# Kernel tuning notes

Hardware: AMD Instinct MI355X
Metric: run time of the kernel (lower is better)

The kernel has to match this reference:

```python
import jax, jax.numpy as jnp
import numpy as np
from jax import lax

WINDOW = 40          # plan.window_size
E = 8                # len(plan.expand_feature)
F = 64               # len(plan.feature)
OUT_CH = 128
KERNEL = 5
ALPHA = 0.01         # leaky_relu_alpha
N_LABEL = 1


def time_conv(x, conv_size):
    """x: [N, T, F] -> [N, WINDOW, 5*E] sliding-window stats over first E features."""
    N, T, _ = x.shape
    begin = T - (conv_size + WINDOW - 1)
    xe = x[:, :, :E]                                             # [N, T, E]
    idx = begin + jnp.arange(WINDOW)[:, None] + jnp.arange(conv_size)[None, :]  # [W, C]
    win = xe[:, idx, :]                                          # [N, W, C, E]
    _mean = win.mean(axis=2)                                     # [N, W, E]
    _std = jnp.std(win, axis=2, ddof=1)                          # torch.std is unbiased
    _max = win.max(axis=2)
    _min = win.min(axis=2)
    # rank of last timestep of each window, cross-sectionally over stocks (dim 0)
    last = xe[:, begin + conv_size - 1: begin + conv_size - 1 + WINDOW, :]  # [N, W, E]
    order = jnp.argsort(-last, axis=0)
    rank = jnp.argsort(order, axis=0).astype(x.dtype) / N        # [N, W, E]
    return jnp.concatenate([_mean, _std, rank, _max, _min], axis=2)  # [N, W, 5E]


def setup_inputs() -> dict:
    key = jax.random.key(0)
    k1, k2, k3, k4, k5 = jax.random.split(key, 5)
    N, T = 8000, 64
    in_ch = F + 10 * E  # 144
    x = jax.random.normal(k1, (N, T, F), dtype=jnp.float32)
    conv_w = jax.random.normal(k2, (OUT_CH, in_ch, KERNEL), dtype=jnp.float32) * 0.05
    conv_b = jax.random.normal(k3, (OUT_CH,), dtype=jnp.float32) * 0.05
    lin_in = WINDOW + 1 - KERNEL  # 36
    lin_w = jax.random.normal(k4, (N_LABEL, lin_in), dtype=jnp.float32) * 0.1
    lin_b = jax.random.normal(k5, (N_LABEL,), dtype=jnp.float32) * 0.1
    return {"x": x, "conv_w": conv_w, "conv_b": conv_b, "lin_w": lin_w, "lin_b": lin_b}


def reference(x, conv_w, conv_b, lin_w, lin_b):
    week_x = time_conv(x, conv_size=5)     # [N, W, 5E]
    month_x = time_conv(x, conv_size=20)   # [N, W, 5E]
    xc = jnp.concatenate([x[:, -WINDOW:, :], week_x, month_x], axis=2)  # [N, W, F+10E]
    cnn_x = jnp.transpose(xc, (0, 2, 1))   # [N, C, W]
    part = lax.conv_general_dilated(cnn_x, conv_w, window_strides=(1,),
                                    padding='VALID',
                                    dimension_numbers=('NCH', 'OIH', 'NCH'))
    part = part + conv_b[None, :, None]    # [N, OUT_CH, W+1-K]
    h = part[:, -1, :]                     # last output channel, [N, W+1-K]
    h = jnp.where(h >= 0, h, ALPHA * h)    # leaky relu
    return h @ lin_w.T + lin_b             # [N, N_LABEL]
```

## Files before the change

kernel.cpp:

```cpp
#include <hip/hip_runtime.h>
#include <math.h>

#define NS    8000
#define TT    64
#define FF    64
#define EE    8
#define WIN   40
#define TR    59
#define NBINS 8192

#define XET_SZ  (8*59*8000)
#define RNK_SZ  (8*40*8000)

__global__ __launch_bounds__(256) void k0(const float* __restrict__ x,
                                          const float* __restrict__ cw,
                                          float* __restrict__ xeT,
                                          float* __restrict__ uraw) {
    int n = blockIdx.x * 256 + threadIdx.x;
    int r = blockIdx.y;
    if (n >= NS) return;
    const float* row = x + (size_t)n * (TT * FF) + (5 + r) * FF;
    float4 a = *(const float4*)(row);
    float4 b = *(const float4*)(row + 4);
    xeT[(0 * TR + r) * NS + n] = a.x;
    xeT[(1 * TR + r) * NS + n] = a.y;
    xeT[(2 * TR + r) * NS + n] = a.z;
    xeT[(3 * TR + r) * NS + n] = a.w;
    xeT[(4 * TR + r) * NS + n] = b.x;
    xeT[(5 * TR + r) * NS + n] = b.y;
    xeT[(6 * TR + r) * NS + n] = b.z;
    xeT[(7 * TR + r) * NS + n] = b.w;

    if (r >= 19) {
        const int w = r - 19;
        const float* W = cw + 127 * 144 * 5;
        float4 v[16];
        v[0] = a; v[1] = b;
#pragma unroll
        for (int q = 2; q < 16; q++) v[q] = *(const float4*)(row + 4 * q);
        float acc0 = 0.f, acc1 = 0.f, acc2 = 0.f, acc3 = 0.f, acc4 = 0.f;
#pragma unroll
        for (int q = 0; q < 16; q++) {
            const float* Wq = W + (4 * q) * 5;
            acc0 += v[q].x * Wq[0]  + v[q].y * Wq[5]  + v[q].z * Wq[10] + v[q].w * Wq[15];
            acc1 += v[q].x * Wq[1]  + v[q].y * Wq[6]  + v[q].z * Wq[11] + v[q].w * Wq[16];
            acc2 += v[q].x * Wq[2]  + v[q].y * Wq[7]  + v[q].z * Wq[12] + v[q].w * Wq[17];
            acc3 += v[q].x * Wq[3]  + v[q].y * Wq[8]  + v[q].z * Wq[13] + v[q].w * Wq[18];
            acc4 += v[q].x * Wq[4]  + v[q].y * Wq[9]  + v[q].z * Wq[14] + v[q].w * Wq[19];
        }
        float* o = uraw + ((size_t)n * WIN + w) * 5;
        o[0] = acc0; o[1] = acc1; o[2] = acc2; o[3] = acc3; o[4] = acc4;
    }
}

__device__ __forceinline__ int binOf(float v) {
    int b = (int)((v + 4.0f) * 1024.0f);
    b = b < 0 ? 0 : b;
    return b > (NBINS - 1) ? (NBINS - 1) : b;
}

__device__ __forceinline__ unsigned long long keyOf(float v, unsigned idx) {
    unsigned s = __float_as_uint(v);
    unsigned m = (s & 0x80000000u) ? (~s) : (s | 0x80000000u);
    unsigned md = ~m;
    return ((unsigned long long)md << 13) | idx;
}

__global__ __launch_bounds__(1024) void k_rank(const float* __restrict__ xeT,
                                               float* __restrict__ rankT) {
    const int w = blockIdx.x;
    const int e = blockIdx.y;
    __shared__ unsigned hist[NBINS];
    __shared__ unsigned basev[NBINS];
    __shared__ unsigned long long sk[NS];
    __shared__ unsigned wsum[16];

    const int tid  = threadIdx.x;
    const int lane = tid & 63;
    const int wid  = tid >> 6;
    const float* col = xeT + ((size_t)e * TR + (19 + w)) * NS;

    float val[8];
#pragma unroll
    for (int i = 0; i < 8; i++) {
        int idx = tid + i * 1024;
        val[i] = (idx < NS) ? col[idx] : 0.0f;
    }
#pragma unroll
    for (int j = 0; j < 8; j++) hist[tid + j * 1024] = 0;
    __syncthreads();

#pragma unroll
    for (int i = 0; i < 8; i++) {
        int idx = tid + i * 1024;
        if (idx < NS) atomicAdd(&hist[binOf(val[i])], 1u);
    }
    __syncthreads();

    unsigned h[8];
#pragma unroll
    for (int j = 0; j < 8; j++) h[j] = hist[8 * tid + j];
    unsigned cs = 0;
#pragma unroll
    for (int j = 0; j < 8; j++) cs += h[j];
    unsigned sc = cs;
#pragma unroll
    for (int d = 1; d < 64; d <<= 1) {
        unsigned t2 = __shfl_up(sc, d);
        if (lane >= d) sc += t2;
    }
    if (lane == 63) wsum[wid] = sc;
    __syncthreads();
    unsigned woff = 0;
    for (int i = 0; i < wid; i++) woff += wsum[i];
    unsigned bsum = woff + (sc - cs);
#pragma unroll
    for (int j = 0; j < 8; j++) {
        int b = 8 * tid + j;
        unsigned bv = NS - bsum - h[j];
        basev[b] = bv;
        hist[b]  = bv;
        bsum += h[j];
    }
    __syncthreads();

#pragma unroll
    for (int i = 0; i < 8; i++) {
        int idx = tid + i * 1024;
        if (idx < NS) {
            int b = binOf(val[i]);
            unsigned p = atomicAdd(&hist[b], 1u);
            sk[p] = keyOf(val[i], (unsigned)idx);
        }
    }
    __syncthreads();

    float* outp = rankT + ((size_t)e * WIN + w) * NS;
#pragma unroll 1
    for (int i = 0; i < 8; i++) {
        int p = tid + i * 1024;
        if (p < NS) {
            unsigned long long k64 = sk[p];
            unsigned md = (unsigned)(k64 >> 13);
            unsigned m  = ~md;
            unsigned s  = (m & 0x80000000u) ? (m ^ 0x80000000u) : (~m);
            float v = __uint_as_float(s);
            int b = binOf(v);
            unsigned lo = basev[b];
            unsigned hi = (b == 0) ? NS : basev[b - 1];
            unsigned c = 0;
            for (unsigned q = lo; q < hi; q++) c += (sk[q] < k64);
            outp[k64 & 8191u] = (float)(basev[b] + c) * (1.0f / 8000.0f);
        }
    }
}

__global__ __launch_bounds__(256) void k_der_final(const float* __restrict__ cw,
                                                   const float* __restrict__ xeT,
                                                   const float* __restrict__ rankT,
                                                   const float* __restrict__ uraw,
                                                   const float* __restrict__ cb,
                                                   const float* __restrict__ lw,
                                                   const float* __restrict__ lb,
                                                   float* __restrict__ outp) {
    __shared__ float red[8][32][37];
    const int tid = threadIdx.x;
    const int e   = tid >> 5;
    const int nl  = tid & 31;
    const int n0  = blockIdx.x * 32;
    const int n   = n0 + nl;
    const float* W = cw + 127 * 144 * 5;

    float wm5[5], wsd5[5], wrk[5], wmx5[5], wmn5[5], wm20[5], wsd20[5], wmx20[5], wmn20[5];
#pragma unroll
    for (int k = 0; k < 5; k++) {
        wm5[k]   = W[(64  + e) * 5 + k];
        wsd5[k]  = W[(72  + e) * 5 + k];
        wrk[k]   = W[(80  + e) * 5 + k] + W[(120 + e) * 5 + k];
        wmx5[k]  = W[(88  + e) * 5 + k];
        wmn5[k]  = W[(96  + e) * 5 + k];
        wm20[k]  = W[(104 + e) * 5 + k];
        wsd20[k] = W[(112 + e) * 5 + k];
        wmx20[k] = W[(128 + e) * 5 + k];
        wmn20[k] = W[(136 + e) * 5 + k];
    }

    float gder[36];
#pragma unroll
    for (int j = 0; j < 36; j++) gder[j] = 0.0f;

    const float* col = xeT + (size_t)e * TR * NS + n;
    const float* rkp = rankT + (size_t)e * WIN * NS + n;

    float ring[20];
#pragma unroll
    for (int r = 0; r < 19; r++) ring[r] = col[(size_t)r * NS];

#pragma unroll
    for (int w = 0; w < WIN; w++) {
        ring[(w + 19) % 20] = col[(size_t)(w + 19) * NS];
        float s20 = 0.f, mn20 = ring[0], mx20 = ring[0];
#pragma unroll
        for (int i = 0; i < 20; i++) {
            float v = ring[i];
            s20 += v; mn20 = fminf(mn20, v); mx20 = fmaxf(mx20, v);
        }
        float m20 = s20 * (1.0f / 20.0f);
        float d20 = 0.f;
#pragma unroll
        for (int i = 0; i < 20; i++) { float t = ring[i] - m20; d20 += t * t; }
        float sd20 = sqrtf(d20 * (1.0f / 19.0f));

        float s5 = 0.f, mn5 = ring[(w + 15) % 20], mx5 = mn5;
#pragma unroll
        for (int i = 15; i < 20; i++) {
            float v = ring[(w + i) % 20];
            s5 += v; mn5 = fminf(mn5, v); mx5 = fmaxf(mx5, v);
        }
        float m5 = s5 * 0.2f;
        float d5 = 0.f;
#pragma unroll
        for (int i = 15; i < 20; i++) {
            float t = ring[(w + i) % 20] - m5; d5 += t * t;
        }
        float sd5 = sqrtf(d5 * 0.25f);

        float rk = rkp[(size_t)w * NS];

#pragma unroll
        for (int k = 0; k < 5; k++) {
            int j = w - k;
            if (j >= 0 && j < 36) {
                float uk;
                uk  = m5   * wm5[k];
                uk += sd5  * wsd5[k];
                uk += rk   * wrk[k];
                uk += mx5  * wmx5[k];
                uk += mn5  * wmn5[k];
                uk += m20  * wm20[k];
                uk += sd20 * wsd20[k];
                uk += mx20 * wmx20[k];
                uk += mn20 * wmn20[k];
                gder[j] += uk;
            }
        }
    }

#pragma unroll
    for (int j = 0; j < 36; j++) red[e][nl][j] = gder[j];
    __syncthreads();

    for (int p = tid; p < 32 * 36; p += 256) {
        int nl2 = p / 36, j = p - nl2 * 36;
        float sum = 0.f;
#pragma unroll
        for (int e2 = 0; e2 < 8; e2++) sum += red[e2][nl2][j];
        red[0][nl2][j] = sum;
    }
    __syncthreads();

    if (tid < 32) {
        const float* ur = uraw + (size_t)n * (WIN * 5);
        float b127 = cb[127];
        float acc = lb[0];
#pragma unroll
        for (int j = 0; j < 36; j++) {
            float g = b127 + red[0][tid][j];
#pragma unroll
            for (int k = 0; k < 5; k++) g += ur[(j + k) * 5 + k];
            g = (g >= 0.0f) ? g : 0.01f * g;
            acc += g * lw[j];
        }
        outp[n] = acc;
    }
}

extern "C" void kernel_launch(void* const* d_in, const int* in_sizes, int n_in,
                              void* d_out, int out_size, void* d_ws, size_t ws_size,
                              hipStream_t stream) {
    const float* x  = (const float*)d_in[0];
    const float* cw = (const float*)d_in[1];
    const float* cb = (const float*)d_in[2];
    const float* lw = (const float*)d_in[3];
    const float* lb = (const float*)d_in[4];
    float* outp = (float*)d_out;

    float* ws    = (float*)d_ws;
    float* xeT   = ws;
    float* rankT = ws + XET_SZ;
    float* uraw  = ws + XET_SZ + RNK_SZ;

    k0<<<dim3(32, 59), 256, 0, stream>>>(x, cw, xeT, uraw);
    k_rank<<<dim3(WIN, EE), 1024, 0, stream>>>(xeT, rankT);
    k_der_final<<<250, 256, 0, stream>>>(cw, xeT, rankT, uraw, cb, lw, lb, outp);
}
```

Baseline: 247.6 us.

## Split derived-feature windows across threads and shrink rank histogram shared memory

The final kernel now splits each stock/feature's 40 windows across four thread groups of 10 windows each. This doubles the block count and threads, and partial sums are reduced through shared memory. The rank kernel halves its histogram bins and reuses the post-scatter histogram as bin bounds, dropping the separate base array to cut shared memory. The trade-offs are redundant ring reloads per split and longer in-bin linear scans from coarser bins.

```diff
diff --git a/kernel.cpp b/kernel.cpp
--- a/kernel.cpp
+++ b/kernel.cpp
@@ -7,7 +7,7 @@
 #define EE    8
 #define WIN   40
 #define TR    59
-#define NBINS 8192
+#define NBINS 4096
 
 #define XET_SZ  (8*59*8000)
 #define RNK_SZ  (8*40*8000)
@@ -54,7 +54,7 @@
 }
 
 __device__ __forceinline__ int binOf(float v) {
-    int b = (int)((v + 4.0f) * 1024.0f);
+    int b = (int)((v + 4.0f) * 512.0f);
     b = b < 0 ? 0 : b;
     return b > (NBINS - 1) ? (NBINS - 1) : b;
 }
@@ -70,8 +70,7 @@
                                                float* __restrict__ rankT) {
     const int w = blockIdx.x;
     const int e = blockIdx.y;
-    __shared__ unsigned hist[NBINS];
-    __shared__ unsigned basev[NBINS];
+    __shared__ unsigned hist[NBINS + 1];
     __shared__ unsigned long long sk[NS];
     __shared__ unsigned wsum[16];
 
@@ -87,7 +86,8 @@
         val[i] = (idx < NS) ? col[idx] : 0.0f;
     }
 #pragma unroll
-    for (int j = 0; j < 8; j++) hist[tid + j * 1024] = 0;
+    for (int j = 0; j < 4; j++) hist[tid + j * 1024] = 0;
+    if (tid == 0) hist[NBINS] = 0;
     __syncthreads();
 
 #pragma unroll
@@ -97,12 +97,10 @@
     }
     __syncthreads();
 
-    unsigned h[8];
-#pragma unroll
-    for (int j = 0; j < 8; j++) h[j] = hist[8 * tid + j];
-    unsigned cs = 0;
-#pragma unroll
-    for (int j = 0; j < 8; j++) cs += h[j];
+    unsigned h[4];
+#pragma unroll
+    for (int j = 0; j < 4; j++) h[j] = hist[4 * tid + j];
+    unsigned cs = h[0] + h[1] + h[2] + h[3];
     unsigned sc = cs;
 #pragma unroll
     for (int d = 1; d < 64; d <<= 1) {
@@ -115,11 +113,9 @@
     for (int i = 0; i < wid; i++) woff += wsum[i];
     unsigned bsum = woff + (sc - cs);
 #pragma unroll
-    for (int j = 0; j < 8; j++) {
-        int b = 8 * tid + j;
-        unsigned bv = NS - bsum - h[j];
-        basev[b] = bv;
-        hist[b]  = bv;
+    for (int j = 0; j < 4; j++) {
+        int b = 4 * tid + j;
+        hist[b] = NS - bsum - h[j];
         bsum += h[j];
     }
     __syncthreads();
@@ -146,16 +142,16 @@
             unsigned s  = (m & 0x80000000u) ? (m ^ 0x80000000u) : (~m);
             float v = __uint_as_float(s);
             int b = binOf(v);
-            unsigned lo = basev[b];
-            unsigned hi = (b == 0) ? NS : basev[b - 1];
+            unsigned lo = hist[b + 1];
+            unsigned hi = hist[b];
             unsigned c = 0;
             for (unsigned q = lo; q < hi; q++) c += (sk[q] < k64);
-            outp[k64 & 8191u] = (float)(basev[b] + c) * (1.0f / 8000.0f);
-        }
-    }
-}
-
-__global__ __launch_bounds__(256) void k_der_final(const float* __restrict__ cw,
+            outp[k64 & 8191u] = (float)(lo + c) * (1.0f / 8000.0f);
+        }
+    }
+}
+
+__global__ __launch_bounds__(512) void k_der_final(const float* __restrict__ cw,
                                                    const float* __restrict__ xeT,
                                                    const float* __restrict__ rankT,
                                                    const float* __restrict__ uraw,
@@ -163,12 +159,16 @@
                                                    const float* __restrict__ lw,
                                                    const float* __restrict__ lb,
                                                    float* __restrict__ outp) {
-    __shared__ float red[8][32][37];
+    __shared__ float red[32][16][15];
+    __shared__ float fin[16][37];
     const int tid = threadIdx.x;
-    const int e   = tid >> 5;
-    const int nl  = tid & 31;
-    const int n0  = blockIdx.x * 32;
+    const int nl  = tid & 15;
+    const int e   = (tid >> 4) & 7;
+    const int q4  = tid >> 7;
+    const int g   = tid >> 4;
+    const int n0  = blockIdx.x * 16;
     const int n   = n0 + nl;
+    const int w0  = q4 * 10;
     const float* W = cw + 127 * 144 * 5;
 
     float wm5[5], wsd5[5], wrk[5], wmx5[5], wmn5[5], wm20[5], wsd20[5], wmx20[5], wmn20[5];
@@ -185,51 +185,51 @@
         wmn20[k] = W[(136 + e) * 5 + k];
     }
 
-    float gder[36];
-#pragma unroll
-    for (int j = 0; j < 36; j++) gder[j] = 0.0f;
-
-    const float* col = xeT + (size_t)e * TR * NS + n;
-    const float* rkp = rankT + (size_t)e * WIN * NS + n;
+    float gl[14];
+#pragma unroll
+    for (int j = 0; j < 14; j++) gl[j] = 0.0f;
+
+    const float* col = xeT + ((size_t)e * TR + w0) * NS + n;
+    const float* rkp = rankT + ((size_t)e * WIN + w0) * NS + n;
 
     float ring[20];
 #pragma unroll
     for (int r = 0; r < 19; r++) ring[r] = col[(size_t)r * NS];
 
 #pragma unroll
-    for (int w = 0; w < WIN; w++) {
-        ring[(w + 19) % 20] = col[(size_t)(w + 19) * NS];
+    for (int i = 0; i < 10; i++) {
+        ring[(i + 19) % 20] = col[(size_t)(i + 19) * NS];
         float s20 = 0.f, mn20 = ring[0], mx20 = ring[0];
 #pragma unroll
-        for (int i = 0; i < 20; i++) {
-            float v = ring[i];
+        for (int t = 0; t < 20; t++) {
+            float v = ring[t];
             s20 += v; mn20 = fminf(mn20, v); mx20 = fmaxf(mx20, v);
         }
         float m20 = s20 * (1.0f / 20.0f);
         float d20 = 0.f;
 #pragma unroll
-        for (int i = 0; i < 20; i++) { float t = ring[i] - m20; d20 += t * t; }
+        for (int t = 0; t < 20; t++) { float d = ring[t] - m20; d20 += d * d; }
         float sd20 = sqrtf(d20 * (1.0f / 19.0f));
 
-        float s5 = 0.f, mn5 = ring[(w + 15) % 20], mx5 = mn5;
-#pragma unroll
-        for (int i = 15; i < 20; i++) {
-            float v = ring[(w + i) % 20];
+        float s5 = 0.f, mn5 = ring[(i + 15) % 20], mx5 = mn5;
+#pragma unroll
+        for (int t = 15; t < 20; t++) {
+            float v = ring[(i + t) % 20];
             s5 += v; mn5 = fminf(mn5, v); mx5 = fmaxf(mx5, v);
         }
         float m5 = s5 * 0.2f;
         float d5 = 0.f;
 #pragma unroll
-        for (int i = 15; i < 20; i++) {
-            float t = ring[(w + i) % 20] - m5; d5 += t * t;
+        for (int t = 15; t < 20; t++) {
+            float d = ring[(i + t) % 20] - m5; d5 += d * d;
         }
         float sd5 = sqrtf(d5 * 0.25f);
 
-        float rk = rkp[(size_t)w * NS];
+        float rk = rkp[(size_t)i * NS];
 
 #pragma unroll
         for (int k = 0; k < 5; k++) {
-            int j = w - k;
+            int j = w0 + i - k;
             if (j >= 0 && j < 36) {
                 float uk;
                 uk  = m5   * wm5[k];
@@ -241,35 +241,41 @@
                 uk += sd20 * wsd20[k];
                 uk += mx20 * wmx20[k];
                 uk += mn20 * wmn20[k];
-                gder[j] += uk;
+                gl[i - k + 4] += uk;
             }
         }
     }
 
 #pragma unroll
-    for (int j = 0; j < 36; j++) red[e][nl][j] = gder[j];
-    __syncthreads();
-
-    for (int p = tid; p < 32 * 36; p += 256) {
+    for (int jj = 0; jj < 14; jj++) red[g][nl][jj] = gl[jj];
+    __syncthreads();
+
+    for (int p = tid; p < 16 * 36; p += 512) {
         int nl2 = p / 36, j = p - nl2 * 36;
-        float sum = 0.f;
-#pragma unroll
-        for (int e2 = 0; e2 < 8; e2++) sum += red[e2][nl2][j];
-        red[0][nl2][j] = sum;
-    }
-    __syncthreads();
-
-    if (tid < 32) {
+        float s = 0.f;
+#pragma unroll
+        for (int qq = 0; qq < 4; qq++) {
+            int lq = j - 10 * qq + 4;
+            if (lq >= 0 && lq < 14) {
+#pragma unroll
+                for (int e2 = 0; e2 < 8; e2++) s += red[qq * 8 + e2][nl2][lq];
+            }
+        }
+        fin[nl2][j] = s;
+    }
+    __syncthreads();
+
+    if (tid < 16) {
         const float* ur = uraw + (size_t)n * (WIN * 5);
         float b127 = cb[127];
         float acc = lb[0];
 #pragma unroll
         for (int j = 0; j < 36; j++) {
-            float g = b127 + red[0][tid][j];
-#pragma unroll
-            for (int k = 0; k < 5; k++) g += ur[(j + k) * 5 + k];
-            g = (g >= 0.0f) ? g : 0.01f * g;
-            acc += g * lw[j];
+            float gsum = b127 + fin[tid][j];
+#pragma unroll
+            for (int k = 0; k < 5; k++) gsum += ur[(j + k) * 5 + k];
+            gsum = (gsum >= 0.0f) ? gsum : 0.01f * gsum;
+            acc += gsum * lw[j];
         }
         outp[n] = acc;
     }
@@ -292,5 +298,5 @@
 
     k0<<<dim3(32, 59), 256, 0, stream>>>(x, cw, xeT, uraw);
     k_rank<<<dim3(WIN, EE), 1024, 0, stream>>>(xeT, rankT);
-    k_der_final<<<250, 256, 0, stream>>>(cw, xeT, rankT, uraw, cb, lw, lb, outp);
-}
+    k_der_final<<<500, 512, 0, stream>>>(cw, xeT, rankT, uraw, cb, lw, lb, outp);
+}
```

Measured after the change: 246.1 us. No clear change (-0.6%).
